# Performance work log

Measured on AMD Instinct MI355X. Metric: run time of the kernel, lower is better.

The kernel has to match this reference:

```python
import jax, jax.numpy as jnp
import numpy as np

EPS = 1e-08

def setup_inputs() -> dict:
    key = jax.random.key(0)
    kH, kF, kQ, kK, kV = jax.random.split(key, 5)
    B, N, d = 8192, 16, 512
    H = jax.random.normal(kH, (B, N, d), dtype=jnp.float32)
    F_raw = jax.random.uniform(kF, (B, N), dtype=jnp.float32)
    F = F_raw / jnp.sum(F_raw, axis=-1, keepdims=True)  # fractions sum to 1
    s = 1.0 / np.sqrt(d)
    W_Q = jax.random.normal(kQ, (d, d), dtype=jnp.float32) * s
    W_K = jax.random.normal(kK, (d, d), dtype=jnp.float32) * s
    W_V = jax.random.normal(kV, (d, d), dtype=jnp.float32) * s
    return {"H": H, "F": F, "W_Q": W_Q, "W_K": W_K, "W_V": W_V}

def reference(H, F, W_Q, W_K, W_V):
    d = H.shape[-1]
    scale = jnp.asarray(d, H.dtype) ** 0.5
    # nn.Linear(d, d, bias=False): y = x @ W.T
    Q = jnp.einsum('bnd,ed->bne', H, W_Q)
    K = jnp.einsum('bnd,ed->bne', H, W_K)
    V = jnp.einsum('bnd,ed->bne', H, W_V)
    scores = jnp.einsum('bqd,bkd->bqk', Q, K) / scale  # [B,N,N]
    scores = scores + jnp.log(F + EPS)[:, None, :]      # fraction bias over keys
    alpha = jax.nn.softmax(scores, axis=-1)
    h_attn = jnp.einsum('bqk,bkd->bqd', alpha, V)
    h_out = H + h_attn                                  # residual
    h_poly = jnp.einsum('bn,bnd->bd', F, h_out)         # fraction-weighted pool
    return h_poly
```

## Files before the change

kernel.cpp:

```cpp
#include <hip/hip_runtime.h>

typedef __bf16 bf16x8 __attribute__((ext_vector_type(8)));
typedef float f32x4 __attribute__((ext_vector_type(4)));

__device__ __forceinline__ unsigned short f2bf(float f) {
    unsigned int u = __builtin_bit_cast(unsigned int, f);
    u += 0x7fffu + ((u >> 16) & 1u);
    return (unsigned short)(u >> 16);
}
__device__ __forceinline__ float bf2f(unsigned short u) {
    return __builtin_bit_cast(float, (unsigned)u << 16);
}

__device__ __forceinline__ unsigned swz1k(unsigned byte) {
    return byte ^ ((byte >> 6) & 0x70u);
}

__device__ __forceinline__ void bar_lgkm() {
    asm volatile("s_waitcnt lgkmcnt(0)\n\ts_barrier" ::: "memory");
}

__global__ __launch_bounds__(256) void prep_kernel(
    const float* __restrict__ Wq, const float* __restrict__ Wk,
    const float* __restrict__ Wv, unsigned short* __restrict__ Pc,
    unsigned short* __restrict__ Wvb)
{
    int b = blockIdx.x;
    if (b < 1024) {
        int j0 = (b >> 4) * 8;
        int kc = b & 15;
        int jloc = threadIdx.x >> 5;
        int t = threadIdx.x & 31;
        int j = j0 + jloc, d = kc * 32 + t;
        float acc = 0.f;
        #pragma unroll 8
        for (int e = 0; e < 512; ++e)
            acc = fmaf(Wk[e * 512 + j], Wq[e * 512 + d], acc);
        Pc[((kc * 512) + j) * 32 + t] = f2bf(acc);
    } else {
        int i = (b - 1024) * 256 + (int)threadIdx.x;
        Wvb[i] = f2bf(Wv[i]);
    }
}

__global__ __launch_bounds__(512, 1) void attn_main_kernel(
    const float* __restrict__ H, const float* __restrict__ F,
    const unsigned short* __restrict__ Pc,
    float* __restrict__ out, unsigned short* __restrict__ g_ws)
{
    extern __shared__ char smem[];
    char* HBF = smem;
    char* TBF = smem + 65536;
    float* wbuf = (float*)(smem + 131072);
    float* FL   = (float*)(smem + 131328);
    float* LFL  = (float*)(smem + 131584);

    const int tid = threadIdx.x;
    const int wv = tid >> 6;
    const int ln = tid & 63;
    const int rl = ln & 15;
    const int kg = ln >> 4;
    const long long gr0 = (long long)blockIdx.x * 64;

    float fval = 0.f;
    if (tid < 64) fval = F[blockIdx.x * 64 + tid];

    const float4* src = (const float4*)(H + gr0 * 512);
    float4 hreg[16];
    #pragma unroll
    for (int rep = 0; rep < 8; ++rep)
        hreg[rep] = src[(rep * 8 + wv) * 128 + ln];
    #pragma unroll
    for (int rep = 0; rep < 8; ++rep)
        hreg[8 + rep] = src[(rep * 8 + wv) * 128 + 64 + ln];

    if (tid < 64) {
        FL[tid] = fval;
        LFL[tid] = logf(fval + 1e-8f);
    }

    #pragma unroll
    for (int rep = 0; rep < 8; ++rep) {
        ushort4 bv;
        bv.x = f2bf(hreg[rep].x); bv.y = f2bf(hreg[rep].y);
        bv.z = f2bf(hreg[rep].z); bv.w = f2bf(hreg[rep].w);
        unsigned byte = (unsigned)(rep * 8 + wv) * 1024u + (unsigned)ln * 8u;
        *(ushort4*)(HBF + swz1k(byte)) = bv;
    }

    const unsigned short* bptr = Pc + ((wv * 64 + rl) * 32 + kg * 8);

    bf16x8 st0[4], st1[4], st2[4];
    #pragma unroll
    for (int jj = 0; jj < 4; ++jj) st0[jj] = *(const bf16x8*)(bptr + 0 * 16384 + jj * 512);
    #pragma unroll
    for (int jj = 0; jj < 4; ++jj) st1[jj] = *(const bf16x8*)(bptr + 1 * 16384 + jj * 512);
    #pragma unroll
    for (int jj = 0; jj < 4; ++jj) st2[jj] = *(const bf16x8*)(bptr + 2 * 16384 + jj * 512);

    f32x4 acc[4][4];
    #pragma unroll
    for (int i = 0; i < 4; ++i)
        #pragma unroll
        for (int jj = 0; jj < 4; ++jj)
            acc[i][jj] = f32x4{0.f, 0.f, 0.f, 0.f};

    bar_lgkm();

    #pragma unroll
    for (int kc = 0; kc < 8; ++kc) {
        bf16x8 bn[4];
        #pragma unroll
        for (int jj = 0; jj < 4; ++jj)
            bn[jj] = *(const bf16x8*)(bptr + (kc + 3) * 16384 + jj * 512);
        bf16x8 a[4];
        #pragma unroll
        for (int i = 0; i < 4; ++i) {
            unsigned off = (unsigned)(i * 16 + rl) * 1024u + (unsigned)kc * 64u + (unsigned)kg * 16u;
            a[i] = *(bf16x8*)(HBF + swz1k(off));
        }
        #pragma unroll
        for (int i = 0; i < 4; ++i)
            #pragma unroll
            for (int jj = 0; jj < 4; ++jj)
                acc[i][jj] = __builtin_amdgcn_mfma_f32_16x16x32_bf16(a[i], st0[jj], acc[i][jj], 0, 0, 0);
        #pragma unroll
        for (int jj = 0; jj < 4; ++jj) { st0[jj] = st1[jj]; st1[jj] = st2[jj]; st2[jj] = bn[jj]; }
    }

    #pragma unroll
    for (int rep = 0; rep < 8; ++rep) {
        ushort4 bv;
        bv.x = f2bf(hreg[8 + rep].x); bv.y = f2bf(hreg[8 + rep].y);
        bv.z = f2bf(hreg[8 + rep].z); bv.w = f2bf(hreg[8 + rep].w);
        unsigned byte = (unsigned)(rep * 8 + wv) * 1024u + (unsigned)(64 + ln) * 8u;
        *(ushort4*)(HBF + swz1k(byte)) = bv;
    }
    bar_lgkm();

    #pragma unroll
    for (int kc = 8; kc < 16; ++kc) {
        bf16x8 bn[4];
        if (kc < 13) {
            #pragma unroll
            for (int jj = 0; jj < 4; ++jj)
                bn[jj] = *(const bf16x8*)(bptr + (kc + 3) * 16384 + jj * 512);
        }
        bf16x8 a[4];
        #pragma unroll
        for (int i = 0; i < 4; ++i) {
            unsigned off = (unsigned)(i * 16 + rl) * 1024u + (unsigned)kc * 64u + (unsigned)kg * 16u;
            a[i] = *(bf16x8*)(HBF + swz1k(off));
        }
        #pragma unroll
        for (int i = 0; i < 4; ++i)
            #pragma unroll
            for (int jj = 0; jj < 4; ++jj)
                acc[i][jj] = __builtin_amdgcn_mfma_f32_16x16x32_bf16(a[i], st0[jj], acc[i][jj], 0, 0, 0);
        #pragma unroll
        for (int jj = 0; jj < 4; ++jj) { st0[jj] = st1[jj]; st1[jj] = st2[jj]; st2[jj] = bn[jj]; }
    }

    #pragma unroll
    for (int i = 0; i < 4; ++i)
        #pragma unroll
        for (int jj = 0; jj < 4; ++jj)
            #pragma unroll
            for (int p = 0; p < 4; ++p) {
                unsigned row = (unsigned)(i * 16 + kg * 4 + p);
                unsigned col = (unsigned)(wv * 64 + jj * 16 + rl);
                *(unsigned short*)(TBF + swz1k(row * 1024u + col * 2u)) = f2bf(acc[i][jj][p]);
            }
    bar_lgkm();

    if (wv < 4) {
        f32x4 sc = f32x4{0.f, 0.f, 0.f, 0.f};
        #pragma unroll
        for (int kc = 0; kc < 16; ++kc) {
            unsigned off = (unsigned)(wv * 16 + rl) * 1024u + (unsigned)kc * 64u + (unsigned)kg * 16u;
            bf16x8 aT = *(bf16x8*)(TBF + swz1k(off));
            bf16x8 bH = *(bf16x8*)(HBF + swz1k(off));
            sc = __builtin_amdgcn_mfma_f32_16x16x32_bf16(aT, bH, sc, 0, 0, 0);
        }
        float bias = LFL[wv * 16 + rl];
        float alpha[4];
        #pragma unroll
        for (int p = 0; p < 4; ++p) {
            float s = sc[p] * 0.044194173824159216f + bias;
            float m = s;
            m = fmaxf(m, __shfl_xor(m, 8));
            m = fmaxf(m, __shfl_xor(m, 4));
            m = fmaxf(m, __shfl_xor(m, 2));
            m = fmaxf(m, __shfl_xor(m, 1));
            float e = expf(s - m);
            float sum = e;
            sum += __shfl_xor(sum, 8);
            sum += __shfl_xor(sum, 4);
            sum += __shfl_xor(sum, 2);
            sum += __shfl_xor(sum, 1);
            alpha[p] = e / sum;
        }
        float part = 0.f;
        #pragma unroll
        for (int p = 0; p < 4; ++p) part += FL[wv * 16 + kg * 4 + p] * alpha[p];
        part += __shfl_xor(part, 16);
        part += __shfl_xor(part, 32);
        if (ln < 16) wbuf[wv * 16 + ln] = part;
    } else {
        int bb = wv - 4;
        const long long Bg = (long long)blockIdx.x * 4 + bb;
        int d0 = ln * 8;
        float o[8];
        #pragma unroll
        for (int q = 0; q < 8; ++q) o[q] = 0.f;
        #pragma unroll
        for (int k = 0; k < 16; ++k) {
            unsigned off = (unsigned)(bb * 16 + k) * 1024u + (unsigned)d0 * 2u;
            ushort4 h0 = *(ushort4*)(HBF + swz1k(off));
            ushort4 h1 = *(ushort4*)(HBF + swz1k(off + 8u));
            float fk = FL[bb * 16 + k];
            o[0] = fmaf(fk, bf2f(h0.x), o[0]); o[1] = fmaf(fk, bf2f(h0.y), o[1]);
            o[2] = fmaf(fk, bf2f(h0.z), o[2]); o[3] = fmaf(fk, bf2f(h0.w), o[3]);
            o[4] = fmaf(fk, bf2f(h1.x), o[4]); o[5] = fmaf(fk, bf2f(h1.y), o[5]);
            o[6] = fmaf(fk, bf2f(h1.z), o[6]); o[7] = fmaf(fk, bf2f(h1.w), o[7]);
        }
        float4 oa; oa.x = o[0]; oa.y = o[1]; oa.z = o[2]; oa.w = o[3];
        float4 ob; ob.x = o[4]; ob.y = o[5]; ob.z = o[6]; ob.w = o[7];
        *(float4*)(out + Bg * 512 + d0) = oa;
        *(float4*)(out + Bg * 512 + d0 + 4) = ob;
    }
    bar_lgkm();

    {
        int bb = wv >> 1, dh = wv & 1;
        const long long Bg = (long long)blockIdx.x * 4 + bb;
        int d0 = dh * 256 + ln * 4;
        float g[4];
        #pragma unroll
        for (int q = 0; q < 4; ++q) g[q] = 0.f;
        #pragma unroll
        for (int k = 0; k < 16; ++k) {
            unsigned off = (unsigned)(bb * 16 + k) * 1024u + (unsigned)d0 * 2u;
            ushort4 h = *(ushort4*)(HBF + swz1k(off));
            float wk = wbuf[bb * 16 + k];
            g[0] = fmaf(wk, bf2f(h.x), g[0]); g[1] = fmaf(wk, bf2f(h.y), g[1]);
            g[2] = fmaf(wk, bf2f(h.z), g[2]); g[3] = fmaf(wk, bf2f(h.w), g[3]);
        }
        ushort4 g4; g4.x = f2bf(g[0]); g4.y = f2bf(g[1]); g4.z = f2bf(g[2]); g4.w = f2bf(g[3]);
        *(ushort4*)(g_ws + Bg * 512 + d0) = g4;
    }
}

__global__ __launch_bounds__(256) void out_gemm_kernel(
    const unsigned short* __restrict__ g_ws,
    const unsigned short* __restrict__ Wvb,
    float* __restrict__ out)
{
    extern __shared__ char smem[];
    const int tid = threadIdx.x;
    const int wv = tid >> 6, ln = tid & 63;
    const int rl = ln & 15, kg = ln >> 4;
    const long long r0 = (long long)blockIdx.x * 32;
    {
        const uint4* src = (const uint4*)(g_ws + r0 * 512);
        #pragma unroll
        for (int q = 0; q < 8; ++q) {
            int idx = q * 256 + tid;
            *(uint4*)(smem + swz1k((unsigned)idx * 16u)) = src[idx];
        }
    }
    __syncthreads();
    f32x4 acc[2][8];
    #pragma unroll
    for (int i = 0; i < 2; ++i)
        #pragma unroll
        for (int jj = 0; jj < 8; ++jj)
            acc[i][jj] = f32x4{0.f, 0.f, 0.f, 0.f};
    for (int kc = 0; kc < 16; ++kc) {
        bf16x8 a[2];
        #pragma unroll
        for (int i = 0; i < 2; ++i) {
            unsigned off = (unsigned)(i * 16 + rl) * 1024u + (unsigned)kc * 64u + (unsigned)kg * 16u;
            a[i] = *(bf16x8*)(smem + swz1k(off));
        }
        bf16x8 bfr[8];
        #pragma unroll
        for (int jj = 0; jj < 8; ++jj) {
            int n = wv * 128 + jj * 16 + rl;
            bfr[jj] = *(const bf16x8*)(Wvb + n * 512 + kc * 32 + kg * 8);
        }
        #pragma unroll
        for (int i = 0; i < 2; ++i)
            #pragma unroll
            for (int jj = 0; jj < 8; ++jj)
                acc[i][jj] = __builtin_amdgcn_mfma_f32_16x16x32_bf16(a[i], bfr[jj], acc[i][jj], 0, 0, 0);
    }
    #pragma unroll
    for (int i = 0; i < 2; ++i)
        #pragma unroll
        for (int jj = 0; jj < 8; ++jj)
            #pragma unroll
            for (int p = 0; p < 4; ++p) {
                int row = i * 16 + kg * 4 + p;
                int col = wv * 128 + jj * 16 + rl;
                out[(r0 + row) * 512 + col] += acc[i][jj][p];
            }
}

extern "C" void kernel_launch(void* const* d_in, const int* in_sizes, int n_in,
                              void* d_out, int out_size, void* d_ws, size_t ws_size,
                              hipStream_t stream)
{
    const float* H  = (const float*)d_in[0];
    const float* F  = (const float*)d_in[1];
    const float* Wq = (const float*)d_in[2];
    const float* Wk = (const float*)d_in[3];
    const float* Wv = (const float*)d_in[4];
    float* out = (float*)d_out;

    unsigned short* Pc  = (unsigned short*)d_ws;
    unsigned short* Wvb = Pc + 262144;
    unsigned short* g   = Wvb + 262144;
    (void)in_sizes; (void)n_in; (void)out_size; (void)ws_size;

    hipLaunchKernelGGL(prep_kernel, dim3(2048), dim3(256), 0, stream, Wq, Wk, Wv, Pc, Wvb);
    hipLaunchKernelGGL(attn_main_kernel, dim3(2048), dim3(512), 131840, stream, H, F, Pc, out, g);
    hipLaunchKernelGGL(out_gemm_kernel, dim3(256), dim3(256), 32768, stream, g, Wvb, out);
}
```

Before: 209.7 us.

## Make attention kernel persistent over four tiles with register double-buffered H prefetch

The main attention kernel now launches 512 blocks, each processing four 64-row tiles in sequence. Each block prefetches the next tile's H into a second register set while the current tile's MFMA work runs, replacing the earlier split of the H load into two halves within a single tile. The aim is to hide HBM latency for H behind compute, since at one block per CU there is otherwise little overlap. The cost is doubled register use for H buffers (which may cause spills) and only 512 blocks to spread across the CUs.

```diff
diff --git a/kernel.cpp b/kernel.cpp
--- a/kernel.cpp
+++ b/kernel.cpp
@@ -43,52 +43,29 @@
     }
 }
 
-__global__ __launch_bounds__(512, 1) void attn_main_kernel(
-    const float* __restrict__ H, const float* __restrict__ F,
-    const unsigned short* __restrict__ Pc,
-    float* __restrict__ out, unsigned short* __restrict__ g_ws)
-{
-    extern __shared__ char smem[];
-    char* HBF = smem;
-    char* TBF = smem + 65536;
-    float* wbuf = (float*)(smem + 131072);
-    float* FL   = (float*)(smem + 131328);
-    float* LFL  = (float*)(smem + 131584);
-
-    const int tid = threadIdx.x;
-    const int wv = tid >> 6;
-    const int ln = tid & 63;
-    const int rl = ln & 15;
-    const int kg = ln >> 4;
-    const long long gr0 = (long long)blockIdx.x * 64;
-
-    float fval = 0.f;
-    if (tid < 64) fval = F[blockIdx.x * 64 + tid];
-
-    const float4* src = (const float4*)(H + gr0 * 512);
-    float4 hreg[16];
-    #pragma unroll
-    for (int rep = 0; rep < 8; ++rep)
-        hreg[rep] = src[(rep * 8 + wv) * 128 + ln];
-    #pragma unroll
-    for (int rep = 0; rep < 8; ++rep)
-        hreg[8 + rep] = src[(rep * 8 + wv) * 128 + 64 + ln];
-
-    if (tid < 64) {
-        FL[tid] = fval;
-        LFL[tid] = logf(fval + 1e-8f);
-    }
-
-    #pragma unroll
-    for (int rep = 0; rep < 8; ++rep) {
+__device__ __forceinline__ void do_tile(
+    int t, long long blk, bool pref,
+    float4 (&cur)[16], float4 (&nxt)[16],
+    const float* __restrict__ H, const unsigned short* __restrict__ Pc,
+    float* __restrict__ out, unsigned short* __restrict__ g_ws,
+    char* HBF, char* TBF, float* wbuf, float* FL, float* LFL,
+    int tid, int wv, int ln, int rl, int kg)
+{
+    const long long gb0 = blk * 16 + t * 4;
+    const int fb = t * 64;
+    const unsigned short* bptr = Pc + ((wv * 64 + rl) * 32 + kg * 8);
+
+    bar_lgkm();
+
+    #pragma unroll
+    for (int rep = 0; rep < 16; ++rep) {
+        int idx = rep * 512 + tid;
         ushort4 bv;
-        bv.x = f2bf(hreg[rep].x); bv.y = f2bf(hreg[rep].y);
-        bv.z = f2bf(hreg[rep].z); bv.w = f2bf(hreg[rep].w);
-        unsigned byte = (unsigned)(rep * 8 + wv) * 1024u + (unsigned)ln * 8u;
+        bv.x = f2bf(cur[rep].x); bv.y = f2bf(cur[rep].y);
+        bv.z = f2bf(cur[rep].z); bv.w = f2bf(cur[rep].w);
+        unsigned byte = (unsigned)(idx >> 7) * 1024u + (unsigned)(idx & 127) * 8u;
         *(ushort4*)(HBF + swz1k(byte)) = bv;
     }
-
-    const unsigned short* bptr = Pc + ((wv * 64 + rl) * 32 + kg * 8);
 
     bf16x8 st0[4], st1[4], st2[4];
     #pragma unroll
@@ -108,7 +85,7 @@
     bar_lgkm();
 
     #pragma unroll
-    for (int kc = 0; kc < 8; ++kc) {
+    for (int kc = 0; kc < 13; ++kc) {
         bf16x8 bn[4];
         #pragma unroll
         for (int jj = 0; jj < 4; ++jj)
@@ -128,28 +105,18 @@
         for (int jj = 0; jj < 4; ++jj) { st0[jj] = st1[jj]; st1[jj] = st2[jj]; st2[jj] = bn[jj]; }
     }
 
-    #pragma unroll
-    for (int rep = 0; rep < 8; ++rep) {
-        ushort4 bv;
-        bv.x = f2bf(hreg[8 + rep].x); bv.y = f2bf(hreg[8 + rep].y);
-        bv.z = f2bf(hreg[8 + rep].z); bv.w = f2bf(hreg[8 + rep].w);
-        unsigned byte = (unsigned)(rep * 8 + wv) * 1024u + (unsigned)(64 + ln) * 8u;
-        *(ushort4*)(HBF + swz1k(byte)) = bv;
-    }
-    bar_lgkm();
-
-    #pragma unroll
-    for (int kc = 8; kc < 16; ++kc) {
-        bf16x8 bn[4];
-        if (kc < 13) {
-            #pragma unroll
-            for (int jj = 0; jj < 4; ++jj)
-                bn[jj] = *(const bf16x8*)(bptr + (kc + 3) * 16384 + jj * 512);
-        }
+    if (pref) {
+        const float4* nsrc = (const float4*)(H + (gb0 + 4) * 8192LL);
+        #pragma unroll
+        for (int rep = 0; rep < 16; ++rep)
+            nxt[rep] = nsrc[rep * 512 + tid];
+    }
+
+    {
         bf16x8 a[4];
         #pragma unroll
         for (int i = 0; i < 4; ++i) {
-            unsigned off = (unsigned)(i * 16 + rl) * 1024u + (unsigned)kc * 64u + (unsigned)kg * 16u;
+            unsigned off = (unsigned)(i * 16 + rl) * 1024u + 13u * 64u + (unsigned)kg * 16u;
             a[i] = *(bf16x8*)(HBF + swz1k(off));
         }
         #pragma unroll
@@ -158,7 +125,25 @@
             for (int jj = 0; jj < 4; ++jj)
                 acc[i][jj] = __builtin_amdgcn_mfma_f32_16x16x32_bf16(a[i], st0[jj], acc[i][jj], 0, 0, 0);
         #pragma unroll
-        for (int jj = 0; jj < 4; ++jj) { st0[jj] = st1[jj]; st1[jj] = st2[jj]; st2[jj] = bn[jj]; }
+        for (int i = 0; i < 4; ++i) {
+            unsigned off = (unsigned)(i * 16 + rl) * 1024u + 14u * 64u + (unsigned)kg * 16u;
+            a[i] = *(bf16x8*)(HBF + swz1k(off));
+        }
+        #pragma unroll
+        for (int i = 0; i < 4; ++i)
+            #pragma unroll
+            for (int jj = 0; jj < 4; ++jj)
+                acc[i][jj] = __builtin_amdgcn_mfma_f32_16x16x32_bf16(a[i], st1[jj], acc[i][jj], 0, 0, 0);
+        #pragma unroll
+        for (int i = 0; i < 4; ++i) {
+            unsigned off = (unsigned)(i * 16 + rl) * 1024u + 15u * 64u + (unsigned)kg * 16u;
+            a[i] = *(bf16x8*)(HBF + swz1k(off));
+        }
+        #pragma unroll
+        for (int i = 0; i < 4; ++i)
+            #pragma unroll
+            for (int jj = 0; jj < 4; ++jj)
+                acc[i][jj] = __builtin_amdgcn_mfma_f32_16x16x32_bf16(a[i], st2[jj], acc[i][jj], 0, 0, 0);
     }
 
     #pragma unroll
@@ -182,7 +167,7 @@
             bf16x8 bH = *(bf16x8*)(HBF + swz1k(off));
             sc = __builtin_amdgcn_mfma_f32_16x16x32_bf16(aT, bH, sc, 0, 0, 0);
         }
-        float bias = LFL[wv * 16 + rl];
+        float bias = LFL[fb + wv * 16 + rl];
         float alpha[4];
         #pragma unroll
         for (int p = 0; p < 4; ++p) {
@@ -202,13 +187,13 @@
         }
         float part = 0.f;
         #pragma unroll
-        for (int p = 0; p < 4; ++p) part += FL[wv * 16 + kg * 4 + p] * alpha[p];
+        for (int p = 0; p < 4; ++p) part += FL[fb + wv * 16 + kg * 4 + p] * alpha[p];
         part += __shfl_xor(part, 16);
         part += __shfl_xor(part, 32);
         if (ln < 16) wbuf[wv * 16 + ln] = part;
     } else {
         int bb = wv - 4;
-        const long long Bg = (long long)blockIdx.x * 4 + bb;
+        const long long Bg = gb0 + bb;
         int d0 = ln * 8;
         float o[8];
         #pragma unroll
@@ -218,7 +203,7 @@
             unsigned off = (unsigned)(bb * 16 + k) * 1024u + (unsigned)d0 * 2u;
             ushort4 h0 = *(ushort4*)(HBF + swz1k(off));
             ushort4 h1 = *(ushort4*)(HBF + swz1k(off + 8u));
-            float fk = FL[bb * 16 + k];
+            float fk = FL[fb + bb * 16 + k];
             o[0] = fmaf(fk, bf2f(h0.x), o[0]); o[1] = fmaf(fk, bf2f(h0.y), o[1]);
             o[2] = fmaf(fk, bf2f(h0.z), o[2]); o[3] = fmaf(fk, bf2f(h0.w), o[3]);
             o[4] = fmaf(fk, bf2f(h1.x), o[4]); o[5] = fmaf(fk, bf2f(h1.y), o[5]);
@@ -233,7 +218,7 @@
 
     {
         int bb = wv >> 1, dh = wv & 1;
-        const long long Bg = (long long)blockIdx.x * 4 + bb;
+        const long long Bg = gb0 + bb;
         int d0 = dh * 256 + ln * 4;
         float g[4];
         #pragma unroll
@@ -249,6 +234,45 @@
         ushort4 g4; g4.x = f2bf(g[0]); g4.y = f2bf(g[1]); g4.z = f2bf(g[2]); g4.w = f2bf(g[3]);
         *(ushort4*)(g_ws + Bg * 512 + d0) = g4;
     }
+}
+
+__global__ __launch_bounds__(512, 1) void attn_main_kernel(
+    const float* __restrict__ H, const float* __restrict__ F,
+    const unsigned short* __restrict__ Pc,
+    float* __restrict__ out, unsigned short* __restrict__ g_ws)
+{
+    extern __shared__ char smem[];
+    char* HBF = smem;
+    char* TBF = smem + 65536;
+    float* wbuf = (float*)(smem + 131072);
+    float* FL   = (float*)(smem + 131328);
+    float* LFL  = (float*)(smem + 132352);
+
+    const int tid = threadIdx.x;
+    const int wv = tid >> 6;
+    const int ln = tid & 63;
+    const int rl = ln & 15;
+    const int kg = ln >> 4;
+    const long long blk = blockIdx.x;
+
+    if (tid < 256) {
+        float fv = F[blk * 256 + tid];
+        FL[tid] = fv;
+        LFL[tid] = logf(fv + 1e-8f);
+    }
+
+    float4 hA[16], hB[16];
+    {
+        const float4* src = (const float4*)(H + blk * 16 * 8192LL);
+        #pragma unroll
+        for (int rep = 0; rep < 16; ++rep)
+            hA[rep] = src[rep * 512 + tid];
+    }
+
+    do_tile(0, blk, true,  hA, hB, H, Pc, out, g_ws, HBF, TBF, wbuf, FL, LFL, tid, wv, ln, rl, kg);
+    do_tile(1, blk, true,  hB, hA, H, Pc, out, g_ws, HBF, TBF, wbuf, FL, LFL, tid, wv, ln, rl, kg);
+    do_tile(2, blk, true,  hA, hB, H, Pc, out, g_ws, HBF, TBF, wbuf, FL, LFL, tid, wv, ln, rl, kg);
+    do_tile(3, blk, false, hB, hA, H, Pc, out, g_ws, HBF, TBF, wbuf, FL, LFL, tid, wv, ln, rl, kg);
 }
 
 __global__ __launch_bounds__(256) void out_gemm_kernel(
@@ -324,6 +348,6 @@
     (void)in_sizes; (void)n_in; (void)out_size; (void)ws_size;
 
     hipLaunchKernelGGL(prep_kernel, dim3(2048), dim3(256), 0, stream, Wq, Wk, Wv, Pc, Wvb);
-    hipLaunchKernelGGL(attn_main_kernel, dim3(2048), dim3(512), 131840, stream, H, F, Pc, out, g);
+    hipLaunchKernelGGL(attn_main_kernel, dim3(512), dim3(512), 133376, stream, H, F, Pc, out, g);
     hipLaunchKernelGGL(out_gemm_kernel, dim3(256), dim3(256), 32768, stream, g, Wvb, out);
 }
```

New measurement: 434.1 us. +107.0%, slower.

## Stream H in quarters overlapped with projection GEMM; split score accumulators

Applied to the files above, without the earlier changes.

H loading and bf16 conversion now happen in four quarter-sized chunks. Each chunk's global loads are issued inside the previous chunk's MFMA loop, replacing the two-half register staging. This is meant to hide global load latency behind the GEMM and to reduce register pressure from holding 16 float4 per thread, at the cost of more barriers. The score MFMA chain is split into four independent accumulators with raised wave priority to break the dependency chain. The F-weighted pooling switches to ushort2 reads over four passes, which may change LDS bank behaviour.

```diff
diff --git a/kernel.cpp b/kernel.cpp
--- a/kernel.cpp
+++ b/kernel.cpp
@@ -43,6 +43,64 @@
     }
 }
 
+__device__ __forceinline__ void issue_quarter(int q, int tid, const float4* hsrc, float4 (&hq)[4]) {
+    #pragma unroll
+    for (int r = 0; r < 4; ++r) {
+        int flat = r * 512 + tid;
+        hq[r] = hsrc[(flat >> 5) * 128 + q * 32 + (flat & 31)];
+    }
+}
+
+__device__ __forceinline__ void convert_quarter(int q, int tid, char* HBF, float4 (&hq)[4]) {
+    #pragma unroll
+    for (int r = 0; r < 4; ++r) {
+        int flat = r * 512 + tid;
+        int row = flat >> 5, ch = flat & 31;
+        ushort4 bv;
+        bv.x = f2bf(hq[r].x); bv.y = f2bf(hq[r].y);
+        bv.z = f2bf(hq[r].z); bv.w = f2bf(hq[r].w);
+        *(ushort4*)(HBF + swz1k((unsigned)row * 1024u + (unsigned)(q * 32 + ch) * 8u)) = bv;
+    }
+}
+
+template<bool PREF>
+__device__ __forceinline__ void gemm_quarter(
+    int kcbase, int tid, int rl, int kg,
+    const unsigned short* bptr, char* HBF,
+    bf16x8 (&st0)[4], bf16x8 (&st1)[4], bf16x8 (&st2)[4],
+    f32x4 (&acc)[4][4],
+    float4 (&hq)[4], const float4* hsrc, int hq_q)
+{
+    #pragma unroll
+    for (int k = 0; k < 4; ++k) {
+        const int kc = kcbase + k;
+        bf16x8 bn[4];
+        if (kc + 3 < 16) {
+            #pragma unroll
+            for (int jj = 0; jj < 4; ++jj)
+                bn[jj] = *(const bf16x8*)(bptr + (kc + 3) * 16384 + jj * 512);
+        }
+        if (PREF && k == 0) {
+            __builtin_amdgcn_sched_barrier(0);
+            issue_quarter(hq_q, tid, hsrc, hq);
+            __builtin_amdgcn_sched_barrier(0);
+        }
+        bf16x8 a[4];
+        #pragma unroll
+        for (int i = 0; i < 4; ++i) {
+            unsigned off = (unsigned)(i * 16 + rl) * 1024u + (unsigned)kc * 64u + (unsigned)kg * 16u;
+            a[i] = *(bf16x8*)(HBF + swz1k(off));
+        }
+        #pragma unroll
+        for (int i = 0; i < 4; ++i)
+            #pragma unroll
+            for (int jj = 0; jj < 4; ++jj)
+                acc[i][jj] = __builtin_amdgcn_mfma_f32_16x16x32_bf16(a[i], st0[jj], acc[i][jj], 0, 0, 0);
+        #pragma unroll
+        for (int jj = 0; jj < 4; ++jj) { st0[jj] = st1[jj]; st1[jj] = st2[jj]; st2[jj] = bn[jj]; }
+    }
+}
+
 __global__ __launch_bounds__(512, 1) void attn_main_kernel(
     const float* __restrict__ H, const float* __restrict__ F,
     const unsigned short* __restrict__ Pc,
@@ -61,43 +119,30 @@
     const int rl = ln & 15;
     const int kg = ln >> 4;
     const long long gr0 = (long long)blockIdx.x * 64;
+    const float4* hsrc = (const float4*)(H + gr0 * 512);
 
     float fval = 0.f;
     if (tid < 64) fval = F[blockIdx.x * 64 + tid];
 
-    const float4* src = (const float4*)(H + gr0 * 512);
-    float4 hreg[16];
-    #pragma unroll
-    for (int rep = 0; rep < 8; ++rep)
-        hreg[rep] = src[(rep * 8 + wv) * 128 + ln];
-    #pragma unroll
-    for (int rep = 0; rep < 8; ++rep)
-        hreg[8 + rep] = src[(rep * 8 + wv) * 128 + 64 + ln];
+    float4 hqA[4], hqB[4];
+    issue_quarter(0, tid, hsrc, hqA);
+
+    const unsigned short* bptr = Pc + ((wv * 64 + rl) * 32 + kg * 8);
+    bf16x8 st0[4], st1[4], st2[4];
+    #pragma unroll
+    for (int jj = 0; jj < 4; ++jj) st0[jj] = *(const bf16x8*)(bptr + 0 * 16384 + jj * 512);
+    #pragma unroll
+    for (int jj = 0; jj < 4; ++jj) st1[jj] = *(const bf16x8*)(bptr + 1 * 16384 + jj * 512);
+    #pragma unroll
+    for (int jj = 0; jj < 4; ++jj) st2[jj] = *(const bf16x8*)(bptr + 2 * 16384 + jj * 512);
+
+    issue_quarter(1, tid, hsrc, hqB);
 
     if (tid < 64) {
         FL[tid] = fval;
         LFL[tid] = logf(fval + 1e-8f);
     }
 
-    #pragma unroll
-    for (int rep = 0; rep < 8; ++rep) {
-        ushort4 bv;
-        bv.x = f2bf(hreg[rep].x); bv.y = f2bf(hreg[rep].y);
-        bv.z = f2bf(hreg[rep].z); bv.w = f2bf(hreg[rep].w);
-        unsigned byte = (unsigned)(rep * 8 + wv) * 1024u + (unsigned)ln * 8u;
-        *(ushort4*)(HBF + swz1k(byte)) = bv;
-    }
-
-    const unsigned short* bptr = Pc + ((wv * 64 + rl) * 32 + kg * 8);
-
-    bf16x8 st0[4], st1[4], st2[4];
-    #pragma unroll
-    for (int jj = 0; jj < 4; ++jj) st0[jj] = *(const bf16x8*)(bptr + 0 * 16384 + jj * 512);
-    #pragma unroll
-    for (int jj = 0; jj < 4; ++jj) st1[jj] = *(const bf16x8*)(bptr + 1 * 16384 + jj * 512);
-    #pragma unroll
-    for (int jj = 0; jj < 4; ++jj) st2[jj] = *(const bf16x8*)(bptr + 2 * 16384 + jj * 512);
-
     f32x4 acc[4][4];
     #pragma unroll
     for (int i = 0; i < 4; ++i)
@@ -105,61 +150,18 @@
         for (int jj = 0; jj < 4; ++jj)
             acc[i][jj] = f32x4{0.f, 0.f, 0.f, 0.f};
 
-    bar_lgkm();
-
-    #pragma unroll
-    for (int kc = 0; kc < 8; ++kc) {
-        bf16x8 bn[4];
-        #pragma unroll
-        for (int jj = 0; jj < 4; ++jj)
-            bn[jj] = *(const bf16x8*)(bptr + (kc + 3) * 16384 + jj * 512);
-        bf16x8 a[4];
-        #pragma unroll
-        for (int i = 0; i < 4; ++i) {
-            unsigned off = (unsigned)(i * 16 + rl) * 1024u + (unsigned)kc * 64u + (unsigned)kg * 16u;
-            a[i] = *(bf16x8*)(HBF + swz1k(off));
-        }
-        #pragma unroll
-        for (int i = 0; i < 4; ++i)
-            #pragma unroll
-            for (int jj = 0; jj < 4; ++jj)
-                acc[i][jj] = __builtin_amdgcn_mfma_f32_16x16x32_bf16(a[i], st0[jj], acc[i][jj], 0, 0, 0);
-        #pragma unroll
-        for (int jj = 0; jj < 4; ++jj) { st0[jj] = st1[jj]; st1[jj] = st2[jj]; st2[jj] = bn[jj]; }
-    }
-
-    #pragma unroll
-    for (int rep = 0; rep < 8; ++rep) {
-        ushort4 bv;
-        bv.x = f2bf(hreg[8 + rep].x); bv.y = f2bf(hreg[8 + rep].y);
-        bv.z = f2bf(hreg[8 + rep].z); bv.w = f2bf(hreg[8 + rep].w);
-        unsigned byte = (unsigned)(rep * 8 + wv) * 1024u + (unsigned)(64 + ln) * 8u;
-        *(ushort4*)(HBF + swz1k(byte)) = bv;
-    }
-    bar_lgkm();
-
-    #pragma unroll
-    for (int kc = 8; kc < 16; ++kc) {
-        bf16x8 bn[4];
-        if (kc < 13) {
-            #pragma unroll
-            for (int jj = 0; jj < 4; ++jj)
-                bn[jj] = *(const bf16x8*)(bptr + (kc + 3) * 16384 + jj * 512);
-        }
-        bf16x8 a[4];
-        #pragma unroll
-        for (int i = 0; i < 4; ++i) {
-            unsigned off = (unsigned)(i * 16 + rl) * 1024u + (unsigned)kc * 64u + (unsigned)kg * 16u;
-            a[i] = *(bf16x8*)(HBF + swz1k(off));
-        }
-        #pragma unroll
-        for (int i = 0; i < 4; ++i)
-            #pragma unroll
-            for (int jj = 0; jj < 4; ++jj)
-                acc[i][jj] = __builtin_amdgcn_mfma_f32_16x16x32_bf16(a[i], st0[jj], acc[i][jj], 0, 0, 0);
-        #pragma unroll
-        for (int jj = 0; jj < 4; ++jj) { st0[jj] = st1[jj]; st1[jj] = st2[jj]; st2[jj] = bn[jj]; }
-    }
+    convert_quarter(0, tid, HBF, hqA);
+    bar_lgkm();
+    gemm_quarter<false>(0, tid, rl, kg, bptr, HBF, st0, st1, st2, acc, hqA, hsrc, 0);
+    convert_quarter(1, tid, HBF, hqB);
+    bar_lgkm();
+    gemm_quarter<true >(4, tid, rl, kg, bptr, HBF, st0, st1, st2, acc, hqA, hsrc, 2);
+    convert_quarter(2, tid, HBF, hqA);
+    bar_lgkm();
+    gemm_quarter<true >(8, tid, rl, kg, bptr, HBF, st0, st1, st2, acc, hqB, hsrc, 3);
+    convert_quarter(3, tid, HBF, hqB);
+    bar_lgkm();
+    gemm_quarter<false>(12, tid, rl, kg, bptr, HBF, st0, st1, st2, acc, hqA, hsrc, 0);
 
     #pragma unroll
     for (int i = 0; i < 4; ++i)
@@ -174,14 +176,23 @@
     bar_lgkm();
 
     if (wv < 4) {
-        f32x4 sc = f32x4{0.f, 0.f, 0.f, 0.f};
+        f32x4 sc0 = f32x4{0.f,0.f,0.f,0.f}, sc1 = sc0, sc2 = sc0, sc3 = sc0;
+        __builtin_amdgcn_s_setprio(1);
         #pragma unroll
         for (int kc = 0; kc < 16; ++kc) {
             unsigned off = (unsigned)(wv * 16 + rl) * 1024u + (unsigned)kc * 64u + (unsigned)kg * 16u;
             bf16x8 aT = *(bf16x8*)(TBF + swz1k(off));
             bf16x8 bH = *(bf16x8*)(HBF + swz1k(off));
-            sc = __builtin_amdgcn_mfma_f32_16x16x32_bf16(aT, bH, sc, 0, 0, 0);
-        }
+            if ((kc & 3) == 0) sc0 = __builtin_amdgcn_mfma_f32_16x16x32_bf16(aT, bH, sc0, 0, 0, 0);
+            else if ((kc & 3) == 1) sc1 = __builtin_amdgcn_mfma_f32_16x16x32_bf16(aT, bH, sc1, 0, 0, 0);
+            else if ((kc & 3) == 2) sc2 = __builtin_amdgcn_mfma_f32_16x16x32_bf16(aT, bH, sc2, 0, 0, 0);
+            else sc3 = __builtin_amdgcn_mfma_f32_16x16x32_bf16(aT, bH, sc3, 0, 0, 0);
+        }
+        __builtin_amdgcn_s_setprio(0);
+        f32x4 sc;
+        #pragma unroll
+        for (int p = 0; p < 4; ++p) sc[p] = (sc0[p] + sc1[p]) + (sc2[p] + sc3[p]);
+
         float bias = LFL[wv * 16 + rl];
         float alpha[4];
         #pragma unroll
@@ -209,25 +220,19 @@
     } else {
         int bb = wv - 4;
         const long long Bg = (long long)blockIdx.x * 4 + bb;
-        int d0 = ln * 8;
-        float o[8];
-        #pragma unroll
-        for (int q = 0; q < 8; ++q) o[q] = 0.f;
-        #pragma unroll
-        for (int k = 0; k < 16; ++k) {
-            unsigned off = (unsigned)(bb * 16 + k) * 1024u + (unsigned)d0 * 2u;
-            ushort4 h0 = *(ushort4*)(HBF + swz1k(off));
-            ushort4 h1 = *(ushort4*)(HBF + swz1k(off + 8u));
-            float fk = FL[bb * 16 + k];
-            o[0] = fmaf(fk, bf2f(h0.x), o[0]); o[1] = fmaf(fk, bf2f(h0.y), o[1]);
-            o[2] = fmaf(fk, bf2f(h0.z), o[2]); o[3] = fmaf(fk, bf2f(h0.w), o[3]);
-            o[4] = fmaf(fk, bf2f(h1.x), o[4]); o[5] = fmaf(fk, bf2f(h1.y), o[5]);
-            o[6] = fmaf(fk, bf2f(h1.z), o[6]); o[7] = fmaf(fk, bf2f(h1.w), o[7]);
-        }
-        float4 oa; oa.x = o[0]; oa.y = o[1]; oa.z = o[2]; oa.w = o[3];
-        float4 ob; ob.x = o[4]; ob.y = o[5]; ob.z = o[6]; ob.w = o[7];
-        *(float4*)(out + Bg * 512 + d0) = oa;
-        *(float4*)(out + Bg * 512 + d0 + 4) = ob;
+        #pragma unroll
+        for (int pass = 0; pass < 4; ++pass) {
+            float a0 = 0.f, a1 = 0.f;
+            #pragma unroll
+            for (int k = 0; k < 16; ++k) {
+                unsigned off = (unsigned)(bb * 16 + k) * 1024u + (unsigned)(pass * 256 + ln * 4);
+                ushort2 h = *(ushort2*)(HBF + swz1k(off));
+                float fk = FL[bb * 16 + k];
+                a0 = fmaf(fk, bf2f(h.x), a0); a1 = fmaf(fk, bf2f(h.y), a1);
+            }
+            float2 o; o.x = a0; o.y = a1;
+            *(float2*)(out + Bg * 512 + pass * 128 + ln * 2) = o;
+        }
     }
     bar_lgkm();
 
```

Result: faster. 196.3 us (-6.4%).
